# Performance work log

Hardware: AMD Instinct MI355X
Metric: run time of the kernel (lower is better)

Reference implementation:

```python
import jax, jax.numpy as jnp
import numpy as np

N_NODES = 100000
N_EDGES = 3200000
IN_DIM, HID_DIM, OUT_DIM = 128, 64, 3


def gcn_conv(x, edge_index, W, b):
    """PyG GCNConv: add self-loops, symmetric deg^{-1/2} normalization,
    linear transform then scatter-sum aggregation, plus bias."""
    n = x.shape[0]
    loop = jnp.arange(n, dtype=edge_index.dtype)
    src = jnp.concatenate([edge_index[0], loop])  # [E+N]
    dst = jnp.concatenate([edge_index[1], loop])
    deg = jax.ops.segment_sum(jnp.ones_like(dst, dtype=x.dtype), dst, num_segments=n)
    dinv = jax.lax.rsqrt(jnp.maximum(deg, 1.0))  # deg >= 1 due to self-loops
    norm = dinv[src] * dinv[dst]                 # [E+N]
    h = x @ W                                    # [N, F_out]
    msgs = h[src] * norm[:, None]                # gather + scale
    out = jax.ops.segment_sum(msgs, dst, num_segments=n)
    return out + b


def setup_inputs() -> dict:
    key = jax.random.key(0)
    k1, k2, k3, k4 = jax.random.split(key, 4)
    x = jax.random.normal(k1, (N_NODES, IN_DIM), dtype=jnp.float32)
    edge_index = jax.random.randint(k2, (2, N_EDGES), 0, N_NODES, dtype=jnp.int64)
    W1 = jax.random.normal(k3, (IN_DIM, HID_DIM), dtype=jnp.float32) * (1.0 / np.sqrt(IN_DIM))
    b1 = jnp.zeros((HID_DIM,), dtype=jnp.float32)
    W2 = jax.random.normal(k4, (HID_DIM, OUT_DIM), dtype=jnp.float32) * (1.0 / np.sqrt(HID_DIM))
    b2 = jnp.zeros((OUT_DIM,), dtype=jnp.float32)
    return {"x": x, "edge_index": edge_index, "W1": W1, "b1": b1, "W2": W2, "b2": b2}


def reference(x, edge_index, W1, b1, W2, b2):
    h = gcn_conv(x, edge_index, W1, b1)
    h = jax.nn.relu(h)
    out = gcn_conv(h, edge_index, W2, b2)
    return out
```

## Files before the change

kernel.cpp:

```cpp
#include <hip/hip_runtime.h>
#include <hip/hip_fp16.h>
#include <cstdint>
#include <cstddef>

#define DIM_IN 128
#define DIM_HID 64
#define MS_TILE 4096
#define OVF_CAP 32768
#define BSH 8
#define BINSZ 256
#define MAXNB 512
#define CAPL 10240

typedef int v2i __attribute__((ext_vector_type(2)));

__global__ __launch_bounds__(512) void k_msplit3(const int* __restrict__ eidx,
                                                 int* __restrict__ binCursor,
                                                 unsigned int* __restrict__ binned,
                                                 int* __restrict__ ovfCnt,
                                                 v2i* __restrict__ ovf,
                                                 int E, int NB, int cap) {
    __shared__ int hist[MAXNB], base[MAXNB];
    __shared__ int stF;
    int t = threadIdx.x;
    if (t == 0) {
        int o = 0;
        for (int j = 1; j < 128; j += 2) o |= eidx[j];
        stF = (o == 0) ? 2 : 1;
    }
    __syncthreads();
    int st = stF;
    int ntiles = (E + MS_TILE - 1) / MS_TILE;

    for (int tile = blockIdx.x; tile < ntiles; tile += gridDim.x) {
        int e0 = tile * MS_TILE;
        int e1 = min(e0 + MS_TILE, E);

        hist[t] = 0;
        __syncthreads();
        for (int e = e0 + t; e < e1; e += 512) {
            int d = (st == 2) ? ((const v2i*)eidx)[E + e].x : eidx[E + e];
            atomicAdd(&hist[d >> BSH], 1);
        }
        __syncthreads();
        if (t < NB && hist[t] > 0) base[t] = atomicAdd(&binCursor[t], hist[t]);
        __syncthreads();
        hist[t] = 0;
        __syncthreads();
        for (int e = e0 + t; e < e1; e += 512) {
            int s, d;
            if (st == 2) {
                s = ((const v2i*)eidx)[e].x;
                d = ((const v2i*)eidx)[E + e].x;
            } else {
                s = eidx[e];
                d = eidx[E + e];
            }
            int b = d >> BSH;
            int r = atomicAdd(&hist[b], 1);
            int local = base[b] + r;
            if (local < cap) {
                binned[(size_t)b * cap + local] =
                    ((unsigned int)s << BSH) | (unsigned int)(d & (BINSZ - 1));
            } else {
                int o = atomicAdd(ovfCnt, 1);
                if (o < OVF_CAP) ovf[o] = (v2i){s, d};
            }
        }
        __syncthreads();
    }
}

__global__ __launch_bounds__(512) void k_binscan(const int* __restrict__ binCursor,
                                                 int* __restrict__ binBase,
                                                 int NB, int cap) {
    __shared__ int sh[512];
    int t = threadIdx.x;
    int v = (t < NB) ? min(binCursor[t], cap) : 0;
    sh[t] = v;
    __syncthreads();
    for (int d = 1; d < 512; d <<= 1) {
        int add = (t >= d) ? sh[t - d] : 0;
        __syncthreads();
        sh[t] += add;
        __syncthreads();
    }
    if (t < NB) binBase[t] = sh[t] - v;
}

__global__ __launch_bounds__(256) void k_fillA(const unsigned int* __restrict__ binned,
                                               const int* __restrict__ binCursor,
                                               const int* __restrict__ binBase,
                                               int* __restrict__ offsets,
                                               int* __restrict__ cursor,
                                               float* __restrict__ dinv,
                                               int* __restrict__ csr,
                                               int cap, int N) {
    __shared__ int hist[BINSZ], scanS[BINSZ], curL[BINSZ];
    __shared__ unsigned int stage[CAPL];
    int b = blockIdx.x;
    int t = threadIdx.x;
    int g0 = b << BSH;
    int g = g0 + t;
    int n = min(binCursor[b], cap);
    const unsigned int* p = binned + (size_t)b * cap;

    hist[t] = 0;
    __syncthreads();
    for (int i = t; i < n; i += 256)
        atomicAdd(&hist[p[i] & (BINSZ - 1)], 1);
    __syncthreads();
    int h = hist[t];
    scanS[t] = h;
    __syncthreads();
    for (int d = 1; d < 256; d <<= 1) {
        int add = (t >= d) ? scanS[t - d] : 0;
        __syncthreads();
        scanS[t] += add;
        __syncthreads();
    }
    int excl = scanS[t] - h;
    int gbase = binBase[b];
    if (g < N) {
        offsets[g] = gbase + excl;
        dinv[g] = rsqrtf((float)(h + 1));
    }
    if (t == 255) offsets[min(g0 + BINSZ, N)] = gbase + scanS[255];

    curL[t] = excl;
    __syncthreads();
    int nl = min(n, CAPL);
    for (int i = t; i < nl; i += 256) {
        unsigned int w = p[i];
        int pos = atomicAdd(&curL[w & (BINSZ - 1)], 1);
        if (pos < CAPL) stage[pos] = w >> BSH;
    }
    __syncthreads();
    if (g < N) cursor[g] = gbase + curL[t];
    for (int i = t; i < nl; i += 256)
        csr[gbase + i] = (int)stage[i];
    __syncthreads();
    for (int i = CAPL + t; i < n; i += 256) {
        unsigned int w = p[i];
        int pos = atomicAdd(&cursor[g0 + (int)(w & (BINSZ - 1))], 1);
        csr[pos] = (int)(w >> BSH);
    }
}

__global__ void k_ovf(const int* __restrict__ ovfCnt, const v2i* __restrict__ ovf,
                      int* __restrict__ cursor, int* __restrict__ csr) {
    int n = min(*ovfCnt, OVF_CAP);
    for (int i = threadIdx.x; i < n; i += 256) {
        v2i e = ovf[i];
        int pos = atomicAdd(&cursor[e.y], 1);
        csr[pos] = e.x;
    }
}

__global__ __launch_bounds__(256) void k_gemm1t(const float* __restrict__ x,
                                                const float* __restrict__ W,
                                                const float* __restrict__ dinv,
                                                __half2* __restrict__ h1, int N) {
    __shared__ float xsT[DIM_IN * 64];
    __shared__ float Ws[DIM_IN * DIM_HID];
    int t = threadIdx.x;
    int row0 = blockIdx.x * 64;

#pragma unroll
    for (int i = 0; i < 8; i++)
        ((float4*)Ws)[t + 256 * i] = ((const float4*)W)[t + 256 * i];

#pragma unroll
    for (int i = 0; i < 8; i++) {
        int idx = t * 8 + i;
        int r = idx >> 5;
        int kc = idx & 31;
        int row = row0 + r;
        float4 v = (row < N) ? ((const float4*)(x + (size_t)row * DIM_IN))[kc]
                             : make_float4(0.f, 0.f, 0.f, 0.f);
        xsT[(4 * kc + 0) * 64 + r] = v.x;
        xsT[(4 * kc + 1) * 64 + r] = v.y;
        xsT[(4 * kc + 2) * 64 + r] = v.z;
        xsT[(4 * kc + 3) * 64 + r] = v.w;
    }
    __syncthreads();

    int c = t & 15;
    int r = t >> 4;
    float acc[4][4] = {};

#pragma unroll 4
    for (int k = 0; k < DIM_IN; k++) {
        float4 xa = *(const float4*)&xsT[k * 64 + 4 * r];
        float4 wb = *(const float4*)&Ws[k * DIM_HID + 4 * c];
#pragma unroll
        for (int i = 0; i < 4; i++) {
            float xi = (i == 0) ? xa.x : (i == 1) ? xa.y : (i == 2) ? xa.z : xa.w;
            acc[i][0] = fmaf(xi, wb.x, acc[i][0]);
            acc[i][1] = fmaf(xi, wb.y, acc[i][1]);
            acc[i][2] = fmaf(xi, wb.z, acc[i][2]);
            acc[i][3] = fmaf(xi, wb.w, acc[i][3]);
        }
    }

#pragma unroll
    for (int i = 0; i < 4; i++) {
        int row = row0 + 4 * r + i;
        if (row < N) {
            float d = dinv[row];
            h1[(size_t)row * 32 + 2 * c] = __floats2half2_rn(acc[i][0] * d, acc[i][1] * d);
            h1[(size_t)row * 32 + 2 * c + 1] = __floats2half2_rn(acc[i][2] * d, acc[i][3] * d);
        }
    }
}

__global__ __launch_bounds__(256) void k_agg1(const __half2* __restrict__ h1,
                                              const int* __restrict__ csr,
                                              const int* __restrict__ offsets,
                                              const float* __restrict__ dinv,
                                              const float* __restrict__ b1,
                                              const float* __restrict__ W2,
                                              float4* __restrict__ h2, int N) {
    int t = threadIdx.x;
    int hl = t & 31;
    int node = blockIdx.x * 8 + (t >> 5);
    if (node >= N) return;

    float di = dinv[node];
    int beg = offsets[node], end = offsets[node + 1];
    __half2 a0 = h1[(size_t)node * 32 + hl];
    __half2 a1 = __floats2half2_rn(0.f, 0.f);

    for (int base = beg; base < end; base += 32) {
        int rem = min(32, end - base);
        int sidx = (hl < rem) ? csr[base + hl] : 0;
        if (rem == 32) {
#pragma unroll
            for (int j0 = 0; j0 < 32; j0 += 8) {
                __half2 v[8];
#pragma unroll
                for (int k = 0; k < 8; k++) {
                    int s = __shfl(sidx, j0 + k, 32);
                    v[k] = h1[(size_t)s * 32 + hl];
                }
#pragma unroll
                for (int k = 0; k < 8; k += 2) {
                    a0 = __hadd2(a0, v[k]);
                    a1 = __hadd2(a1, v[k + 1]);
                }
            }
        } else {
            int j = 0;
            for (; j + 1 < rem; j += 2) {
                int s0 = __shfl(sidx, j, 32);
                int s1 = __shfl(sidx, j + 1, 32);
                a0 = __hadd2(a0, h1[(size_t)s0 * 32 + hl]);
                a1 = __hadd2(a1, h1[(size_t)s1 * 32 + hl]);
            }
            if (j < rem) {
                int s0 = __shfl(sidx, j, 32);
                a0 = __hadd2(a0, h1[(size_t)s0 * 32 + hl]);
            }
        }
    }

    float2 f0 = __half22float2(a0);
    float2 f1 = __half22float2(a1);
    float accx = f0.x + f1.x, accy = f0.y + f1.y;

    float2 bb = ((const float2*)b1)[hl];
    float gx = fmaxf(fmaf(accx, di, bb.x), 0.f);
    float gy = fmaxf(fmaf(accy, di, bb.y), 0.f);

    const float* w0 = W2 + (2 * hl) * 3;
    const float* w1 = W2 + (2 * hl + 1) * 3;
    float v0 = gx * w0[0] + gy * w1[0];
    float v1 = gx * w0[1] + gy * w1[1];
    float v2 = gx * w0[2] + gy * w1[2];
#pragma unroll
    for (int off = 16; off > 0; off >>= 1) {
        v0 += __shfl_xor(v0, off, 64);
        v1 += __shfl_xor(v1, off, 64);
        v2 += __shfl_xor(v2, off, 64);
    }
    if (hl == 0) h2[node] = make_float4(v0 * di, v1 * di, v2 * di, 0.f);
}

__global__ __launch_bounds__(256) void k_agg2(const float4* __restrict__ h2,
                                              const int* __restrict__ csr,
                                              const int* __restrict__ offsets,
                                              const float* __restrict__ dinv,
                                              const float* __restrict__ b2,
                                              float* __restrict__ out, int N) {
    int t = threadIdx.x;
    int l = t & 7;
    int node = blockIdx.x * 32 + (t >> 3);
    if (node >= N) return;

    float di = dinv[node];
    int beg = offsets[node], end = offsets[node + 1];
    float a0 = 0.f, a1 = 0.f, a2 = 0.f;
    for (int e = beg + l; e < end; e += 8) {
        float4 h = h2[csr[e]];
        a0 += h.x;
        a1 += h.y;
        a2 += h.z;
    }
#pragma unroll
    for (int off = 4; off > 0; off >>= 1) {
        a0 += __shfl_xor(a0, off, 8);
        a1 += __shfl_xor(a1, off, 8);
        a2 += __shfl_xor(a2, off, 8);
    }
    if (l == 0) {
        float4 hs = h2[node];
        out[(size_t)node * 3 + 0] = fmaf(a0 + hs.x, di, b2[0]);
        out[(size_t)node * 3 + 1] = fmaf(a1 + hs.y, di, b2[1]);
        out[(size_t)node * 3 + 2] = fmaf(a2 + hs.z, di, b2[2]);
    }
}

extern "C" void kernel_launch(void* const* d_in, const int* in_sizes, int n_in,
                              void* d_out, int out_size, void* d_ws, size_t ws_size,
                              hipStream_t stream) {
    const float* x = (const float*)d_in[0];
    const int* eidx = (const int*)d_in[1];
    const float* W1 = (const float*)d_in[2];
    const float* b1 = (const float*)d_in[3];
    const float* W2 = (const float*)d_in[4];
    const float* b2 = (const float*)d_in[5];
    float* out = (float*)d_out;

    const int N = in_sizes[0] / DIM_IN;
    const int E = in_sizes[1] / 2;
    const int NB = (N + BINSZ - 1) >> BSH;

    char* w = (char*)d_ws;
    size_t off = 0;
    auto carve = [&](size_t bytes) -> char* {
        char* p = w + off;
        off += (bytes + 255) & ~(size_t)255;
        return p;
    };
    int* offsets = (int*)carve((size_t)(N + 1) * 4);
    int* cursor = (int*)carve((size_t)N * 4);
    float* dinv = (float*)carve((size_t)N * 4);
    int* csr = (int*)carve((size_t)E * 4);
    int* binCursor = (int*)carve(MAXNB * 4);
    int* ovfCnt = (int*)carve(16);
    v2i* ovf = (v2i*)carve((size_t)OVF_CAP * 8);
    int* binBase = (int*)carve(MAXNB * 4);
    float4* h2 = (float4*)carve((size_t)N * 16);

    size_t h1_bytes = (size_t)N * DIM_HID * 2;
    int capDes = E / NB + E / NB / 16 + 128;
    size_t binned_des = (size_t)NB * capDes * 4;
    size_t uni_avail = (ws_size > off + 256) ? (ws_size - off - 256) : h1_bytes;
    size_t uni_bytes = binned_des > h1_bytes ? binned_des : h1_bytes;
    if (uni_bytes > uni_avail) uni_bytes = uni_avail > h1_bytes ? uni_avail : h1_bytes;
    char* uni = carve(uni_bytes);
    unsigned int* binned = (unsigned int*)uni;
    __half2* h1 = (__half2*)uni;
    int cap = (int)(uni_bytes / ((size_t)NB * 4));
    if (cap > capDes) cap = capDes;
    if (cap > CAPL) cap = CAPL;

    (void)hipMemsetAsync(binCursor, 0, MAXNB * 4 + 256, stream);

    int ntiles = (E + MS_TILE - 1) / MS_TILE;
    k_msplit3<<<ntiles, 512, 0, stream>>>(eidx, binCursor, binned, ovfCnt, ovf,
                                          E, NB, cap);
    k_binscan<<<1, 512, 0, stream>>>(binCursor, binBase, NB, cap);
    k_fillA<<<NB, 256, 0, stream>>>(binned, binCursor, binBase, offsets, cursor,
                                    dinv, csr, cap, N);
    k_ovf<<<1, 256, 0, stream>>>(ovfCnt, ovf, cursor, csr);

    k_gemm1t<<<(N + 63) / 64, 256, 0, stream>>>(x, W1, dinv, h1, N);
    k_agg1<<<(N + 7) / 8, 256, 0, stream>>>(h1, csr, offsets, dinv, b1, W2, h2, N);
    k_agg2<<<(N + 31) / 32, 256, 0, stream>>>(h2, csr, offsets, dinv, b2, out, N);
}
```

Baseline: 195.6 us.

## Replace global-atomic edge binning with per-tile local sort and segment offsets

The edge bucketing pass now sorts each 4096-edge tile locally in shared memory by destination bin and writes per-tile bin offsets, rather than reserving space with global atomics into fixed-capacity bins with an overflow path. A new reduction kernel totals each bin across tiles, and the CSR fill kernel walks the per-tile segments for its bin. This removes global atomic contention, the memset, the overflow kernel and the capacity limits. In exchange, the fill kernel reads many short scattered segments serially per thread, with uneven work and poor coalescing.

Measured after the change: 218.1 us. +11.5%, slower.

```diff
diff --git a/kernel.cpp b/kernel.cpp
--- a/kernel.cpp
+++ b/kernel.cpp
@@ -6,21 +6,19 @@
 #define DIM_IN 128
 #define DIM_HID 64
 #define MS_TILE 4096
-#define OVF_CAP 32768
 #define BSH 8
 #define BINSZ 256
 #define MAXNB 512
+#define MAXT 1024
 #define CAPL 10240
 
 typedef int v2i __attribute__((ext_vector_type(2)));
 
-__global__ __launch_bounds__(512) void k_msplit3(const int* __restrict__ eidx,
-                                                 int* __restrict__ binCursor,
-                                                 unsigned int* __restrict__ binned,
-                                                 int* __restrict__ ovfCnt,
-                                                 v2i* __restrict__ ovf,
-                                                 int E, int NB, int cap) {
-    __shared__ int hist[MAXNB], base[MAXNB];
+__global__ __launch_bounds__(256) void k_msplit4(const int* __restrict__ eidx,
+                                                 unsigned int* __restrict__ sorted,
+                                                 int* __restrict__ offs,
+                                                 int E, int NB) {
+    __shared__ int hist[MAXNB], scanb[MAXNB], s4[128];
     __shared__ int stF;
     int t = threadIdx.x;
     if (t == 0) {
@@ -28,55 +26,87 @@
         for (int j = 1; j < 128; j += 2) o |= eidx[j];
         stF = (o == 0) ? 2 : 1;
     }
+    hist[t] = 0; hist[t + 256] = 0;
     __syncthreads();
     int st = stF;
-    int ntiles = (E + MS_TILE - 1) / MS_TILE;
-
-    for (int tile = blockIdx.x; tile < ntiles; tile += gridDim.x) {
-        int e0 = tile * MS_TILE;
-        int e1 = min(e0 + MS_TILE, E);
-
-        hist[t] = 0;
-        __syncthreads();
-        for (int e = e0 + t; e < e1; e += 512) {
-            int d = (st == 2) ? ((const v2i*)eidx)[E + e].x : eidx[E + e];
-            atomicAdd(&hist[d >> BSH], 1);
-        }
-        __syncthreads();
-        if (t < NB && hist[t] > 0) base[t] = atomicAdd(&binCursor[t], hist[t]);
-        __syncthreads();
-        hist[t] = 0;
-        __syncthreads();
-        for (int e = e0 + t; e < e1; e += 512) {
+
+    int tile = blockIdx.x;
+    int e0 = tile * MS_TILE;
+    int e1 = min(e0 + MS_TILE, E);
+
+    unsigned int words[16];
+    int bins[16];
+#pragma unroll
+    for (int j = 0; j < 16; j++) {
+        int e = e0 + t + 256 * j;
+        if (e < e1) {
             int s, d;
             if (st == 2) {
-                s = ((const v2i*)eidx)[e].x;
-                d = ((const v2i*)eidx)[E + e].x;
+                v2i a = __builtin_nontemporal_load((const v2i*)eidx + e);
+                v2i b = __builtin_nontemporal_load((const v2i*)eidx + E + e);
+                s = a.x; d = b.x;
             } else {
-                s = eidx[e];
-                d = eidx[E + e];
+                s = __builtin_nontemporal_load(&eidx[e]);
+                d = __builtin_nontemporal_load(&eidx[E + e]);
             }
-            int b = d >> BSH;
-            int r = atomicAdd(&hist[b], 1);
-            int local = base[b] + r;
-            if (local < cap) {
-                binned[(size_t)b * cap + local] =
-                    ((unsigned int)s << BSH) | (unsigned int)(d & (BINSZ - 1));
-            } else {
-                int o = atomicAdd(ovfCnt, 1);
-                if (o < OVF_CAP) ovf[o] = (v2i){s, d};
-            }
-        }
-        __syncthreads();
-    }
-}
-
-__global__ __launch_bounds__(512) void k_binscan(const int* __restrict__ binCursor,
-                                                 int* __restrict__ binBase,
-                                                 int NB, int cap) {
+            words[j] = ((unsigned int)s << BSH) | (unsigned int)(d & (BINSZ - 1));
+            bins[j] = d >> BSH;
+            atomicAdd(&hist[bins[j]], 1);
+        } else {
+            bins[j] = -1;
+        }
+    }
+    __syncthreads();
+    if (t < 128)
+        s4[t] = hist[4 * t] + hist[4 * t + 1] + hist[4 * t + 2] + hist[4 * t + 3];
+    __syncthreads();
+    if (t == 0) {
+        int run = 0;
+        for (int b = 0; b < 128; b++) { int v = s4[b]; s4[b] = run; run += v; }
+    }
+    __syncthreads();
+    if (t < 128) {
+        int r = s4[t];
+#pragma unroll
+        for (int j = 0; j < 4; j++) { scanb[4 * t + j] = r; r += hist[4 * t + j]; }
+    }
+    __syncthreads();
+    for (int b = t; b <= NB; b += 256)
+        offs[(size_t)tile * (NB + 1) + b] = scanb[b];
+    hist[t] = 0; hist[t + 256] = 0;
+    __syncthreads();
+#pragma unroll
+    for (int j = 0; j < 16; j++) {
+        if (bins[j] >= 0) {
+            int r = atomicAdd(&hist[bins[j]], 1);
+            sorted[e0 + scanb[bins[j]] + r] = words[j];
+        }
+    }
+}
+
+__global__ __launch_bounds__(256) void k_binsum(const int* __restrict__ offs,
+                                                int* __restrict__ binTot,
+                                                int ntiles, int NB) {
+    __shared__ int sh[256];
+    int b = blockIdx.x;
+    int t = threadIdx.x;
+    int sum = 0;
+    for (int T = t; T < ntiles; T += 256)
+        sum += offs[(size_t)T * (NB + 1) + b + 1] - offs[(size_t)T * (NB + 1) + b];
+    sh[t] = sum;
+    __syncthreads();
+    for (int d = 128; d > 0; d >>= 1) {
+        if (t < d) sh[t] += sh[t + d];
+        __syncthreads();
+    }
+    if (t == 0) binTot[b] = sh[0];
+}
+
+__global__ __launch_bounds__(512) void k_binscan(const int* __restrict__ binTot,
+                                                 int* __restrict__ binBase, int NB) {
     __shared__ int sh[512];
     int t = threadIdx.x;
-    int v = (t < NB) ? min(binCursor[t], cap) : 0;
+    int v = (t < NB) ? binTot[t] : 0;
     sh[t] = v;
     __syncthreads();
     for (int d = 1; d < 512; d <<= 1) {
@@ -88,28 +118,37 @@
     if (t < NB) binBase[t] = sh[t] - v;
 }
 
-__global__ __launch_bounds__(256) void k_fillA(const unsigned int* __restrict__ binned,
-                                               const int* __restrict__ binCursor,
-                                               const int* __restrict__ binBase,
-                                               int* __restrict__ offsets,
-                                               int* __restrict__ cursor,
-                                               float* __restrict__ dinv,
-                                               int* __restrict__ csr,
-                                               int cap, int N) {
+__global__ __launch_bounds__(256) void k_fillA2(const unsigned int* __restrict__ sorted,
+                                                const int* __restrict__ offs,
+                                                const int* __restrict__ binBase,
+                                                int* __restrict__ offsets,
+                                                float* __restrict__ dinv,
+                                                int* __restrict__ csr,
+                                                int ntiles, int NB, int N) {
+    __shared__ int segLo[MAXT], segHi[MAXT];
     __shared__ int hist[BINSZ], scanS[BINSZ], curL[BINSZ];
     __shared__ unsigned int stage[CAPL];
     int b = blockIdx.x;
     int t = threadIdx.x;
     int g0 = b << BSH;
     int g = g0 + t;
-    int n = min(binCursor[b], cap);
-    const unsigned int* p = binned + (size_t)b * cap;
 
     hist[t] = 0;
     __syncthreads();
-    for (int i = t; i < n; i += 256)
-        atomicAdd(&hist[p[i] & (BINSZ - 1)], 1);
-    __syncthreads();
+    for (int T0 = 0; T0 < ntiles; T0 += MAXT) {
+        int tc = min(MAXT, ntiles - T0);
+        for (int T = t; T < tc; T += 256) {
+            segLo[T] = offs[(size_t)(T0 + T) * (NB + 1) + b];
+            segHi[T] = offs[(size_t)(T0 + T) * (NB + 1) + b + 1];
+        }
+        __syncthreads();
+        for (int T = t; T < tc; T += 256) {
+            const unsigned int* p = sorted + (size_t)(T0 + T) * MS_TILE;
+            for (int i = segLo[T]; i < segHi[T]; i++)
+                atomicAdd(&hist[p[i] & (BINSZ - 1)], 1);
+        }
+        __syncthreads();
+    }
     int h = hist[t];
     scanS[t] = h;
     __syncthreads();
@@ -126,35 +165,30 @@
         dinv[g] = rsqrtf((float)(h + 1));
     }
     if (t == 255) offsets[min(g0 + BINSZ, N)] = gbase + scanS[255];
-
     curL[t] = excl;
     __syncthreads();
-    int nl = min(n, CAPL);
-    for (int i = t; i < nl; i += 256) {
-        unsigned int w = p[i];
-        int pos = atomicAdd(&curL[w & (BINSZ - 1)], 1);
-        if (pos < CAPL) stage[pos] = w >> BSH;
-    }
-    __syncthreads();
-    if (g < N) cursor[g] = gbase + curL[t];
+
+    for (int T0 = 0; T0 < ntiles; T0 += MAXT) {
+        int tc = min(MAXT, ntiles - T0);
+        for (int T = t; T < tc; T += 256) {
+            segLo[T] = offs[(size_t)(T0 + T) * (NB + 1) + b];
+            segHi[T] = offs[(size_t)(T0 + T) * (NB + 1) + b + 1];
+        }
+        __syncthreads();
+        for (int T = t; T < tc; T += 256) {
+            const unsigned int* p = sorted + (size_t)(T0 + T) * MS_TILE;
+            for (int i = segLo[T]; i < segHi[T]; i++) {
+                unsigned int w = p[i];
+                int pos = atomicAdd(&curL[w & (BINSZ - 1)], 1);
+                if (pos < CAPL) stage[pos] = w >> BSH;
+                else csr[gbase + pos] = (int)(w >> BSH);
+            }
+        }
+        __syncthreads();
+    }
+    int nl = min(scanS[255], CAPL);
     for (int i = t; i < nl; i += 256)
         csr[gbase + i] = (int)stage[i];
-    __syncthreads();
-    for (int i = CAPL + t; i < n; i += 256) {
-        unsigned int w = p[i];
-        int pos = atomicAdd(&cursor[g0 + (int)(w & (BINSZ - 1))], 1);
-        csr[pos] = (int)(w >> BSH);
-    }
-}
-
-__global__ void k_ovf(const int* __restrict__ ovfCnt, const v2i* __restrict__ ovf,
-                      int* __restrict__ cursor, int* __restrict__ csr) {
-    int n = min(*ovfCnt, OVF_CAP);
-    for (int i = threadIdx.x; i < n; i += 256) {
-        v2i e = ovf[i];
-        int pos = atomicAdd(&cursor[e.y], 1);
-        csr[pos] = e.x;
-    }
 }
 
 __global__ __launch_bounds__(256) void k_gemm1t(const float* __restrict__ x,
@@ -334,6 +368,7 @@
     const int N = in_sizes[0] / DIM_IN;
     const int E = in_sizes[1] / 2;
     const int NB = (N + BINSZ - 1) >> BSH;
+    const int ntiles = (E + MS_TILE - 1) / MS_TILE;
 
     char* w = (char*)d_ws;
     size_t off = 0;
@@ -343,37 +378,25 @@
         return p;
     };
     int* offsets = (int*)carve((size_t)(N + 1) * 4);
-    int* cursor = (int*)carve((size_t)N * 4);
     float* dinv = (float*)carve((size_t)N * 4);
     int* csr = (int*)carve((size_t)E * 4);
-    int* binCursor = (int*)carve(MAXNB * 4);
-    int* ovfCnt = (int*)carve(16);
-    v2i* ovf = (v2i*)carve((size_t)OVF_CAP * 8);
+    int* offs = (int*)carve((size_t)ntiles * (NB + 1) * 4);
+    int* binTot = (int*)carve(MAXNB * 4);
     int* binBase = (int*)carve(MAXNB * 4);
     float4* h2 = (float4*)carve((size_t)N * 16);
 
     size_t h1_bytes = (size_t)N * DIM_HID * 2;
-    int capDes = E / NB + E / NB / 16 + 128;
-    size_t binned_des = (size_t)NB * capDes * 4;
-    size_t uni_avail = (ws_size > off + 256) ? (ws_size - off - 256) : h1_bytes;
-    size_t uni_bytes = binned_des > h1_bytes ? binned_des : h1_bytes;
-    if (uni_bytes > uni_avail) uni_bytes = uni_avail > h1_bytes ? uni_avail : h1_bytes;
+    size_t sorted_bytes = (size_t)E * 4;
+    size_t uni_bytes = sorted_bytes > h1_bytes ? sorted_bytes : h1_bytes;
     char* uni = carve(uni_bytes);
-    unsigned int* binned = (unsigned int*)uni;
+    unsigned int* sorted = (unsigned int*)uni;
     __half2* h1 = (__half2*)uni;
-    int cap = (int)(uni_bytes / ((size_t)NB * 4));
-    if (cap > capDes) cap = capDes;
-    if (cap > CAPL) cap = CAPL;
-
-    (void)hipMemsetAsync(binCursor, 0, MAXNB * 4 + 256, stream);
-
-    int ntiles = (E + MS_TILE - 1) / MS_TILE;
-    k_msplit3<<<ntiles, 512, 0, stream>>>(eidx, binCursor, binned, ovfCnt, ovf,
-                                          E, NB, cap);
-    k_binscan<<<1, 512, 0, stream>>>(binCursor, binBase, NB, cap);
-    k_fillA<<<NB, 256, 0, stream>>>(binned, binCursor, binBase, offsets, cursor,
-                                    dinv, csr, cap, N);
-    k_ovf<<<1, 256, 0, stream>>>(ovfCnt, ovf, cursor, csr);
+
+    k_msplit4<<<ntiles, 256, 0, stream>>>(eidx, sorted, offs, E, NB);
+    k_binsum<<<NB, 256, 0, stream>>>(offs, binTot, ntiles, NB);
+    k_binscan<<<1, 512, 0, stream>>>(binTot, binBase, NB);
+    k_fillA2<<<NB, 256, 0, stream>>>(sorted, offs, binBase, offsets, dinv, csr,
+                                     ntiles, NB, N);
 
     k_gemm1t<<<(N + 63) / 64, 256, 0, stream>>>(x, W1, dinv, h1, N);
     k_agg1<<<(N + 7) / 8, 256, 0, stream>>>(h1, csr, offsets, dinv, b1, W2, h2, N);
```
